# Optimization experiments

Hardware: AMD Instinct MI355X
Metric: run time of the kernel (lower is better)

## Reference

```python
import jax, jax.numpy as jnp
import numpy as np

# ConvTemporalGraphical (GRIP) forward, eval mode (Dropout = identity).
# All convs are 1x1, i.e. channel-mixing matmuls.

N, V, C_IN, C_OUT, K = 64, 256, 64, 64, 6


def setup_inputs() -> dict:
    key = jax.random.key(0)
    ks = jax.random.split(key, 11)
    x = jax.random.normal(ks[0], (N, C_OUT, V), dtype=jnp.float32)
    xo = jax.random.normal(ks[1], (N, C_IN, V), dtype=jnp.float32)
    A = jax.random.uniform(ks[2], (N, K, V, V), dtype=jnp.float32)
    s = 0.1
    w1 = jax.random.normal(ks[3], (16, 5), dtype=jnp.float32) * s
    b1 = jax.random.normal(ks[4], (16,), dtype=jnp.float32) * s
    w2 = jax.random.normal(ks[5], (32, 16), dtype=jnp.float32) * s
    b2 = jax.random.normal(ks[6], (32,), dtype=jnp.float32) * s
    w3 = jax.random.normal(ks[7], (64, 32), dtype=jnp.float32) * s
    b3 = jax.random.normal(ks[8], (64,), dtype=jnp.float32) * s
    wo = jax.random.normal(ks[9], (C_OUT, C_IN), dtype=jnp.float32) * s
    bo = jax.random.normal(ks[10], (C_OUT,), dtype=jnp.float32) * s
    return {"x": x, "xo": xo, "A": A, "w1": w1, "b1": b1, "w2": w2,
            "b2": b2, "w3": w3, "b3": b3, "wo": wo, "bo": bo}


def reference(x, xo, A, w1, b1, w2, b2, w3, b3, wo, bo):
    # convo: 1x1 Conv1d over channels -> [N, C_OUT, V]
    xo_c = jnp.einsum('niv,oi->nov', xo, wo) + bo[None, :, None]
    # adjmatder on A[:, :5]: 1x1 Conv2d stack 5->16->32->64 (Dropout is eval identity)
    h = jax.nn.relu(jnp.einsum('nivw,oi->novw', A[:, :5], w1) + b1[None, :, None, None])
    h = jax.nn.relu(jnp.einsum('nivw,oi->novw', h, w2) + b2[None, :, None, None])
    A_out = jax.nn.sigmoid(jnp.einsum('nivw,oi->novw', h, w3) + b3[None, :, None, None])
    # neighbor aggregation + sigmoid gating
    posterior_prob = jax.nn.sigmoid(jnp.einsum('ncv,ncvw->ncw', xo_c, A_out))
    return x * posterior_prob, A_out
```

## Files before the change

kernel.cpp:

```cpp
#include <hip/hip_runtime.h>
#include <hip/hip_bf16.h>

#define NV 256
#define NC 64
#define VW 65536
#define NE1 1048576
#define VB 8

typedef __attribute__((ext_vector_type(8))) short bf16x8;
typedef __attribute__((ext_vector_type(16))) float f32x16;
typedef __attribute__((ext_vector_type(2))) unsigned int uint2v;

union fu32 { float f; unsigned int u; };
union U4 { unsigned int u[4]; bf16x8 v8; };

static __device__ __forceinline__ short f2bf(float x) {
    union { __hip_bfloat16 b; short s; } u;
    u.b = __float2bfloat16(x);
    return u.s;
}
static __device__ __forceinline__ unsigned int cvt_pk_bf16(float a, float b) {
    unsigned int r;
    asm("v_cvt_pk_bf16_f32 %0, %1, %2" : "=v"(r) : "v"(a), "v"(b));
    return r;
}

__global__ __launch_bounds__(256) void k1_xoc(
    const float* __restrict__ xo, const float* __restrict__ wo,
    const float* __restrict__ bo, float* __restrict__ xoc)
{
    const int idx = blockIdx.x * 256 + threadIdx.x;
    const int v = idx & 255;
    const int c = (idx >> 8) & 63;
    const int n = idx >> 14;
    const float* xon = xo + (size_t)n * 64 * NV;
    const float* wrow = wo + c * 64;
    float s = bo[c];
#pragma unroll
    for (int i = 0; i < 64; ++i)
        s = fmaf(wrow[i], xon[i * NV + v], s);
    xoc[idx] = s;
}

__global__ __launch_bounds__(256) void k2_mfma(
    const float* __restrict__ A,
    const float* __restrict__ w1, const float* __restrict__ b1,
    const float* __restrict__ w2, const float* __restrict__ b2,
    const float* __restrict__ w3, const float* __restrict__ b3,
    const float* __restrict__ xoc,
    float* __restrict__ Aout, float* __restrict__ post)
{
    __shared__ float xocs[NC][VB];

    const int t    = threadIdx.x;
    const int wt   = t >> 6;
    const int lane = t & 63;
    const int lo   = lane & 31;
    const int hi   = lane >> 5;
    const int vbase = blockIdx.x * VB;
    const int n    = blockIdx.y;
    const int w0   = wt << 6;

    for (int e = t; e < NC * VB; e += 256) {
        const int c = e >> 3, j = e & (VB - 1);
        xocs[c][j] = xoc[(size_t)n * (NC * NV) + c * NV + vbase + j];
    }
    __syncthreads();

    bf16x8 af[2][2];
#pragma unroll
    for (int ct = 0; ct < 2; ++ct)
#pragma unroll
        for (int h = 0; h < 2; ++h) {
            const float* wp = w3 + ((ct << 5) + lo) * 32 + (h << 4) + (hi << 3);
            bf16x8 pk;
#pragma unroll
            for (int e = 0; e < 8; ++e) pk[e] = f2bf(wp[e]);
            af[ct][h] = pk;
        }
    bf16x8 af2;
#pragma unroll
    for (int e = 0; e < 8; ++e) af2[e] = f2bf(w2[lo * 16 + (hi << 3) + e]);

    float gacc[2][16][2];
#pragma unroll
    for (int ct = 0; ct < 2; ++ct)
#pragma unroll
        for (int r = 0; r < 16; ++r) {
            gacc[ct][r][0] = 0.0f;
            gacc[ct][r][1] = 0.0f;
        }

    const float* An  = A    + (size_t)n * 6 * VW;
    float*       Aon = Aout + (size_t)n * NC * VW;
    const float NLOG2E = -1.4426950408889634f;

    const float* ap0 = An + (size_t)vbase * NV + w0 + lane;
    float a0 = ap0[0], a1 = ap0[VW], a2 = ap0[2 * VW],
          a3 = ap0[3 * VW], a4 = ap0[4 * VW];

    for (int vi = 0; vi < VB; ++vi) {
        const int v = vbase + vi;

        const int vn = (vi + 1 < VB) ? (vi + 1) : vi;
        const float* apn = ap0 + (size_t)vn * NV;
        const float na0 = apn[0], na1 = apn[VW], na2 = apn[2 * VW],
                    na3 = apn[3 * VW], na4 = apn[4 * VW];

        unsigned int h1p[8];
#pragma unroll
        for (int m = 0; m < 8; ++m) {
            float sa = b1[2 * m];
            float sb = b1[2 * m + 1];
            sa = fmaf(w1[(2 * m) * 5 + 0], a0, sa);
            sa = fmaf(w1[(2 * m) * 5 + 1], a1, sa);
            sa = fmaf(w1[(2 * m) * 5 + 2], a2, sa);
            sa = fmaf(w1[(2 * m) * 5 + 3], a3, sa);
            sa = fmaf(w1[(2 * m) * 5 + 4], a4, sa);
            sb = fmaf(w1[(2 * m + 1) * 5 + 0], a0, sb);
            sb = fmaf(w1[(2 * m + 1) * 5 + 1], a1, sb);
            sb = fmaf(w1[(2 * m + 1) * 5 + 2], a2, sb);
            sb = fmaf(w1[(2 * m + 1) * 5 + 3], a3, sb);
            sb = fmaf(w1[(2 * m + 1) * 5 + 4], a4, sb);
            h1p[m] = cvt_pk_bf16(fmaxf(sa, 0.0f), fmaxf(sb, 0.0f));
        }

        U4 b1T0, b1T1;
#pragma unroll
        for (int j = 0; j < 4; ++j) {
            uint2v r = __builtin_amdgcn_permlane32_swap(h1p[j], h1p[4 + j],
                                                        false, false);
            b1T0.u[j] = r.x;
            b1T1.u[j] = r.y;
        }
        f32x16 d20, d21;
#pragma unroll
        for (int r = 0; r < 16; ++r) {
            const float bv = b2[(r & 3) + ((r >> 2) << 3) + (hi << 2)];
            d20[r] = bv; d21[r] = bv;
        }
        d20 = __builtin_amdgcn_mfma_f32_32x32x16_bf16(af2, b1T0.v8, d20, 0, 0, 0);
        d21 = __builtin_amdgcn_mfma_f32_32x32x16_bf16(af2, b1T1.v8, d21, 0, 0, 0);

        unsigned int p[8], q[8];
#pragma unroll
        for (int j = 0; j < 8; ++j) {
            p[j] = cvt_pk_bf16(fmaxf(d20[2 * j], 0.0f), fmaxf(d20[2 * j + 1], 0.0f));
            q[j] = cvt_pk_bf16(fmaxf(d21[2 * j], 0.0f), fmaxf(d21[2 * j + 1], 0.0f));
        }
        U4 b3f[2][2];
#pragma unroll
        for (int h = 0; h < 2; ++h) {
            uint2v r02 = __builtin_amdgcn_permlane32_swap(p[4 * h + 0], p[4 * h + 2], false, false);
            uint2v r13 = __builtin_amdgcn_permlane32_swap(p[4 * h + 1], p[4 * h + 3], false, false);
            b3f[0][h].u[0] = r02.x; b3f[0][h].u[2] = r02.y;
            b3f[0][h].u[1] = r13.x; b3f[0][h].u[3] = r13.y;
            uint2v s02 = __builtin_amdgcn_permlane32_swap(q[4 * h + 0], q[4 * h + 2], false, false);
            uint2v s13 = __builtin_amdgcn_permlane32_swap(q[4 * h + 1], q[4 * h + 3], false, false);
            b3f[1][h].u[0] = s02.x; b3f[1][h].u[2] = s02.y;
            b3f[1][h].u[1] = s13.x; b3f[1][h].u[3] = s13.y;
        }

        float* rowp = Aon + (size_t)v * NV + w0 + lane;

#pragma unroll
        for (int ct = 0; ct < 2; ++ct) {
            f32x16 d0, d1;
#pragma unroll
            for (int r = 0; r < 16; ++r) { d0[r] = 0.0f; d1[r] = 0.0f; }
            d0 = __builtin_amdgcn_mfma_f32_32x32x16_bf16(af[ct][0], b3f[0][0].v8, d0, 0, 0, 0);
            d0 = __builtin_amdgcn_mfma_f32_32x32x16_bf16(af[ct][1], b3f[0][1].v8, d0, 0, 0, 0);
            d1 = __builtin_amdgcn_mfma_f32_32x32x16_bf16(af[ct][0], b3f[1][0].v8, d1, 0, 0, 0);
            d1 = __builtin_amdgcn_mfma_f32_32x32x16_bf16(af[ct][1], b3f[1][1].v8, d1, 0, 0, 0);
#pragma unroll
            for (int r = 0; r < 16; ++r) {
                const int cx = (ct << 5) + (r & 3) + ((r >> 2) << 3);
                const int cy = cx + 4;
                fu32 ux, uy, mx, my;
                ux.f = d0[r]; uy.f = d1[r];
                uint2v m = __builtin_amdgcn_permlane32_swap(ux.u, uy.u, false, false);
                mx.u = m.x; my.u = m.y;
                const float vx = __builtin_amdgcn_rcpf(
                    1.0f + __builtin_amdgcn_exp2f(fmaf(mx.f, NLOG2E, b3[cx] * NLOG2E)));
                const float vy = __builtin_amdgcn_rcpf(
                    1.0f + __builtin_amdgcn_exp2f(fmaf(my.f, NLOG2E, b3[cy] * NLOG2E)));
                __builtin_nontemporal_store(vx, rowp + (size_t)cx * VW);
                __builtin_nontemporal_store(vy, rowp + (size_t)cy * VW);
                gacc[ct][r][0] = fmaf(xocs[cx][vi], vx, gacc[ct][r][0]);
                gacc[ct][r][1] = fmaf(xocs[cy][vi], vy, gacc[ct][r][1]);
            }
        }

        a0 = na0; a1 = na1; a2 = na2; a3 = na3; a4 = na4;
    }

    float* pn = post + (size_t)n * (NC * NV) + w0 + lane;
#pragma unroll
    for (int ct = 0; ct < 2; ++ct)
#pragma unroll
        for (int r = 0; r < 16; ++r) {
            const int cx = (ct << 5) + (r & 3) + ((r >> 2) << 3);
            atomicAdd(pn + cx * NV,       gacc[ct][r][0]);
            atomicAdd(pn + (cx + 4) * NV, gacc[ct][r][1]);
        }
}

__global__ __launch_bounds__(256) void k3_gate(
    const float* __restrict__ x, const float* __restrict__ post,
    float* __restrict__ out1)
{
    const int idx = blockIdx.x * 256 + threadIdx.x;
    const float p = 1.0f / (1.0f + __expf(-post[idx]));
    out1[idx] = x[idx] * p;
}

extern "C" void kernel_launch(void* const* d_in, const int* in_sizes, int n_in,
                              void* d_out, int out_size, void* d_ws, size_t ws_size,
                              hipStream_t stream)
{
    const float* x  = (const float*)d_in[0];
    const float* xo = (const float*)d_in[1];
    const float* A  = (const float*)d_in[2];
    const float* w1 = (const float*)d_in[3];
    const float* b1 = (const float*)d_in[4];
    const float* w2 = (const float*)d_in[5];
    const float* b2 = (const float*)d_in[6];
    const float* w3 = (const float*)d_in[7];
    const float* b3 = (const float*)d_in[8];
    const float* wo = (const float*)d_in[9];
    const float* bo = (const float*)d_in[10];

    float* out1 = (float*)d_out;
    float* Aout = (float*)d_out + NE1;

    float* xoc  = (float*)d_ws;
    float* post = (float*)d_ws + NE1;

    hipMemsetAsync(post, 0, (size_t)NE1 * sizeof(float), stream);
    k1_xoc<<<NE1 / 256, 256, 0, stream>>>(xo, wo, bo, xoc);
    k2_mfma<<<dim3(NV / VB, 64), 256, 0, stream>>>(A, w1, b1, w2, b2, w3, b3,
                                                   xoc, Aout, post);
    k3_gate<<<NE1 / 256, 256, 0, stream>>>(x, post, out1);
}
```

Measured before the change: 281.2 us.

## Replace atomic reduction with per-block partial buffers and enlarge v-block

Each k2 block now writes its per-channel aggregation partials to a dedicated slice of a workspace buffer instead of atomically adding into a shared post buffer. The gate kernel then sums the slices. The v-block size grows from 8 to 32, which cuts the number of partial slices and the grid size. This drops the memset and the atomic contention, at the cost of extra partial traffic and lower grid parallelism, and it falls back to atomics if the workspace is too small.

```diff
diff --git a/kernel.cpp b/kernel.cpp
--- a/kernel.cpp
+++ b/kernel.cpp
@@ -5,7 +5,7 @@
 #define NC 64
 #define VW 65536
 #define NE1 1048576
-#define VB 8
+#define VB 32
 
 typedef __attribute__((ext_vector_type(8))) short bf16x8;
 typedef __attribute__((ext_vector_type(16))) float f32x16;
@@ -42,13 +42,14 @@
     xoc[idx] = s;
 }
 
+template <bool USE_PART>
 __global__ __launch_bounds__(256) void k2_mfma(
     const float* __restrict__ A,
     const float* __restrict__ w1, const float* __restrict__ b1,
     const float* __restrict__ w2, const float* __restrict__ b2,
     const float* __restrict__ w3, const float* __restrict__ b3,
     const float* __restrict__ xoc,
-    float* __restrict__ Aout, float* __restrict__ post)
+    float* __restrict__ Aout, float* __restrict__ gout)
 {
     __shared__ float xocs[NC][VB];
 
@@ -62,7 +63,7 @@
     const int w0   = wt << 6;
 
     for (int e = t; e < NC * VB; e += 256) {
-        const int c = e >> 3, j = e & (VB - 1);
+        const int c = e >> 5, j = e & (VB - 1);
         xocs[c][j] = xoc[(size_t)n * (NC * NV) + c * NV + vbase + j];
     }
     __syncthreads();
@@ -194,23 +195,46 @@
         a0 = na0; a1 = na1; a2 = na2; a3 = na3; a4 = na4;
     }
 
-    float* pn = post + (size_t)n * (NC * NV) + w0 + lane;
-#pragma unroll
-    for (int ct = 0; ct < 2; ++ct)
-#pragma unroll
-        for (int r = 0; r < 16; ++r) {
-            const int cx = (ct << 5) + (r & 3) + ((r >> 2) << 3);
-            atomicAdd(pn + cx * NV,       gacc[ct][r][0]);
-            atomicAdd(pn + (cx + 4) * NV, gacc[ct][r][1]);
-        }
-}
-
+    if (USE_PART) {
+        float* gp = gout + (size_t)blockIdx.x * NE1
+                         + (size_t)n * (NC * NV) + w0 + lane;
+#pragma unroll
+        for (int ct = 0; ct < 2; ++ct)
+#pragma unroll
+            for (int r = 0; r < 16; ++r) {
+                const int cx = (ct << 5) + (r & 3) + ((r >> 2) << 3);
+                gp[cx * NV]       = gacc[ct][r][0];
+                gp[(cx + 4) * NV] = gacc[ct][r][1];
+            }
+    } else {
+        float* pn = gout + (size_t)n * (NC * NV) + w0 + lane;
+#pragma unroll
+        for (int ct = 0; ct < 2; ++ct)
+#pragma unroll
+            for (int r = 0; r < 16; ++r) {
+                const int cx = (ct << 5) + (r & 3) + ((r >> 2) << 3);
+                atomicAdd(pn + cx * NV,       gacc[ct][r][0]);
+                atomicAdd(pn + (cx + 4) * NV, gacc[ct][r][1]);
+            }
+    }
+}
+
+template <bool USE_PART>
 __global__ __launch_bounds__(256) void k3_gate(
-    const float* __restrict__ x, const float* __restrict__ post,
+    const float* __restrict__ x, const float* __restrict__ g,
     float* __restrict__ out1)
 {
     const int idx = blockIdx.x * 256 + threadIdx.x;
-    const float p = 1.0f / (1.0f + __expf(-post[idx]));
+    float s;
+    if (USE_PART) {
+        s = g[idx];
+#pragma unroll
+        for (int b = 1; b < NV / VB; ++b)
+            s += g[(size_t)b * NE1 + idx];
+    } else {
+        s = g[idx];
+    }
+    const float p = 1.0f / (1.0f + __expf(-s));
     out1[idx] = x[idx] * p;
 }
 
@@ -234,11 +258,20 @@
     float* Aout = (float*)d_out + NE1;
 
     float* xoc  = (float*)d_ws;
-    float* post = (float*)d_ws + NE1;
-
-    hipMemsetAsync(post, 0, (size_t)NE1 * sizeof(float), stream);
+    float* gbuf = (float*)d_ws + NE1;
+
+    const bool use_part =
+        ws_size >= (size_t)(NE1 + (NV / VB) * NE1) * sizeof(float);
+
     k1_xoc<<<NE1 / 256, 256, 0, stream>>>(xo, wo, bo, xoc);
-    k2_mfma<<<dim3(NV / VB, 64), 256, 0, stream>>>(A, w1, b1, w2, b2, w3, b3,
-                                                   xoc, Aout, post);
-    k3_gate<<<NE1 / 256, 256, 0, stream>>>(x, post, out1);
-}
+    if (use_part) {
+        k2_mfma<true><<<dim3(NV / VB, 64), 256, 0, stream>>>(
+            A, w1, b1, w2, b2, w3, b3, xoc, Aout, gbuf);
+        k3_gate<true><<<NE1 / 256, 256, 0, stream>>>(x, gbuf, out1);
+    } else {
+        hipMemsetAsync(gbuf, 0, (size_t)NE1 * sizeof(float), stream);
+        k2_mfma<false><<<dim3(NV / VB, 64), 256, 0, stream>>>(
+            A, w1, b1, w2, b2, w3, b3, xoc, Aout, gbuf);
+        k3_gate<false><<<NE1 / 256, 256, 0, stream>>>(x, gbuf, out1);
+    }
+}
```

After: 279.9 us. Within noise of the previous version (-0.4%).
